# Kernel optimization log

Hardware: AMD Instinct MI355X
Metric: run time of the kernel (lower is better)

Reference implementation:

```python
import jax, jax.numpy as jnp
import numpy as np

NUM_GRAPHS = 64

def setup_inputs() -> dict:
    key = jax.random.key(0)
    ks = jax.random.split(key, 12)
    N, E, D, H = 100000, 1600000, 128, 128
    s = 0.05  # weight scale for numerical stability
    x = jax.random.normal(ks[0], (N, D), dtype=jnp.float32)
    edge_src = jax.random.randint(ks[1], (E,), 0, N, dtype=jnp.int32)
    edge_dst = jax.random.randint(ks[2], (E,), 0, N, dtype=jnp.int32)
    batch = jnp.sort(jax.random.randint(ks[3], (N,), 0, NUM_GRAPHS, dtype=jnp.int32))
    Wp = jax.random.normal(ks[4], (D, H), dtype=jnp.float32) * s
    bp = jnp.zeros((H,), dtype=jnp.float32)
    Wr = jax.random.normal(ks[5], (4, H, H), dtype=jnp.float32) * s
    br = jnp.zeros((4, H), dtype=jnp.float32)
    Wo0 = jax.random.normal(ks[6], (H + D, H), dtype=jnp.float32) * s
    bo0 = jnp.zeros((H,), dtype=jnp.float32)
    Wo1 = jax.random.normal(ks[7], (H, H), dtype=jnp.float32) * s
    bo1 = jnp.zeros((H,), dtype=jnp.float32)
    return dict(x=x, Wp=Wp, bp=bp, Wr=Wr, br=br, Wo0=Wo0, bo0=bo0, Wo1=Wo1, bo1=bo1,
                edge_src=edge_src, edge_dst=edge_dst, batch=batch)

def reference(x, Wp, bp, Wr, br, Wo0, bo0, Wo1, bo1, edge_src, edge_dst, batch):
    N = x.shape[0]
    # GCN normalization with self-loops: deg[i] = in_degree(i) + 1
    deg = 1.0 + jax.ops.segment_sum(jnp.ones_like(edge_dst, dtype=x.dtype), edge_dst, num_segments=N)
    dis = deg ** -0.5                      # [N]
    enorm = dis[edge_src] * dis[edge_dst]  # [E] edge coefficients
    self_norm = (dis * dis)[:, None]       # [N,1] self-loop coefficient

    def gcn(h, W, b):
        h = h @ W                                              # [N,out]
        msg = h[edge_src] * enorm[:, None]                     # [E,out] gather
        agg = jax.ops.segment_sum(msg, edge_dst, num_segments=N)  # scatter-add
        return agg + h * self_norm + b

    # projection (dropout is identity in this deterministic reference)
    h = jax.nn.relu(gcn(x, Wp, bp))
    # recurrent block, 1 training iteration of 4 layers
    for i in range(4):
        h = jax.nn.relu(gcn(h, Wr[i], br[i]))
    h = jnp.concatenate([h, x], axis=1)    # [N, H+D]
    h = jax.nn.relu(h)
    # output head
    h = jax.nn.relu(gcn(h, Wo0, bo0))
    h = jax.nn.relu(gcn(h, Wo1, bo1))
    # global mean pool over graphs
    sums = jax.ops.segment_sum(h, batch, num_segments=NUM_GRAPHS)
    cnt = jax.ops.segment_sum(jnp.ones((N,), dtype=h.dtype), batch, num_segments=NUM_GRAPHS)
    return sums / jnp.maximum(cnt, 1.0)[:, None]
```

## Files before the change

### kernel.cpp

```cpp
#include <hip/hip_runtime.h>

typedef __attribute__((ext_vector_type(8))) short short8;
typedef __attribute__((ext_vector_type(4))) float f32x4;
typedef __attribute__((ext_vector_type(4))) unsigned short us4;

__device__ __forceinline__ unsigned short f2bf(float f) {
  unsigned int u = __float_as_uint(f);
  u = u + 0x7fffu + ((u >> 16) & 1u);
  return (unsigned short)(u >> 16);
}
__device__ __forceinline__ float bf2f(unsigned short h) {
  return __uint_as_float(((unsigned int)h) << 16);
}
__device__ __forceinline__ int swz(int r, int k) {
  return (((r * 128 + k) * 2) ^ ((r & 7) << 4));
}

__global__ void k_deg(const int* __restrict__ edst, int* __restrict__ degi, int E) {
  int e = blockIdx.x * 256 + threadIdx.x;
  if (e < E) atomicAdd(&degi[edst[e]], 1);
}

__global__ void k_node(const int* __restrict__ degi, int* __restrict__ start,
                       float* __restrict__ dis, int* __restrict__ total, int N) {
  int tid = threadIdx.x;
  int i = blockIdx.x * 256 + tid;
  int d = (i < N) ? degi[i] : 0;
  __shared__ int sd[256];
  sd[tid] = d; __syncthreads();
  #pragma unroll
  for (int off = 1; off < 256; off <<= 1) {
    int v = (tid >= off) ? sd[tid - off] : 0;
    __syncthreads();
    sd[tid] += v;
    __syncthreads();
  }
  __shared__ int sbase;
  if (tid == 255) sbase = atomicAdd(total, sd[255]);
  __syncthreads();
  if (i < N) {
    start[i] = sbase + sd[tid] - d;
    dis[i] = rsqrtf(1.0f + (float)d);
  }
}

__global__ void k_fill(const int* __restrict__ esrc, const int* __restrict__ edst,
                       const int* __restrict__ start, int* __restrict__ cursor,
                       const float* __restrict__ dis, int* __restrict__ col,
                       float* __restrict__ wgt, int E) {
  int e = blockIdx.x * 256 + threadIdx.x;
  if (e >= E) return;
  int d = edst[e], s = esrc[e];
  int p = start[d] + atomicAdd(&cursor[d], 1);
  col[p] = s;
  wgt[p] = dis[s] * dis[d];
}

__global__ void k_wt(const float* __restrict__ Wp, const float* __restrict__ Wr,
                     const float* __restrict__ Wo0, const float* __restrict__ Wo1,
                     unsigned short* __restrict__ Whi, unsigned short* __restrict__ Wlo) {
  int idx = blockIdx.x * 256 + threadIdx.x;
  if (idx >= 8 * 16384) return;
  int m = idx >> 14, rem = idx & 16383;
  int c = rem >> 7, k = rem & 127;
  float v;
  if (m == 0)       v = Wp[k * 128 + c];
  else if (m <= 4)  v = Wr[(m - 1) * 16384 + k * 128 + c];
  else if (m == 5)  v = Wo0[k * 128 + c];
  else if (m == 6)  v = Wo0[(128 + k) * 128 + c];
  else              v = Wo1[k * 128 + c];
  unsigned short hh = f2bf(v);
  Whi[idx] = hh;
  Wlo[idx] = f2bf(v - bf2f(hh));
}

#define AHI_OFF 0
#define ALO_OFF 16384
#define WHI_OFF 32768
#define WLO_OFF 49152

template<bool ACC, bool RELU_A>
__global__ __launch_bounds__(256)
void k_gemm(const float* __restrict__ A, const unsigned short* __restrict__ Whi,
            const unsigned short* __restrict__ Wlo, unsigned short* __restrict__ TB, int N) {
  __shared__ __align__(16) char smem[65536];
  const int tid = threadIdx.x;
  const int grow = blockIdx.x * 64;
  const int cb = blockIdx.y * 64;

  #pragma unroll
  for (int it = 0; it < 4; ++it) {
    int id = it * 256 + tid;
    int r = id >> 4;
    int kp = (id & 15) * 8;
    int ga = grow + r; if (ga > N - 1) ga = N - 1;
    const float* ap = A + (size_t)ga * 128 + kp;
    float4 a0 = *(const float4*)ap;
    float4 a1 = *(const float4*)(ap + 4);
    if (RELU_A) {
      a0.x = fmaxf(a0.x, 0.f); a0.y = fmaxf(a0.y, 0.f); a0.z = fmaxf(a0.z, 0.f); a0.w = fmaxf(a0.w, 0.f);
      a1.x = fmaxf(a1.x, 0.f); a1.y = fmaxf(a1.y, 0.f); a1.z = fmaxf(a1.z, 0.f); a1.w = fmaxf(a1.w, 0.f);
    }
    {
      float fv[8] = {a0.x, a0.y, a0.z, a0.w, a1.x, a1.y, a1.z, a1.w};
      short8 hi, lo;
      #pragma unroll
      for (int q = 0; q < 8; ++q) {
        unsigned short hh = f2bf(fv[q]);
        hi[q] = (short)hh;
        lo[q] = (short)f2bf(fv[q] - bf2f(hh));
      }
      *(short8*)(smem + AHI_OFF + swz(r, kp)) = hi;
      *(short8*)(smem + ALO_OFF + swz(r, kp)) = lo;
    }
    size_t wo = (size_t)(cb + r) * 128 + kp;
    *(short8*)(smem + WHI_OFF + swz(r, kp)) = *(const short8*)(Whi + wo);
    *(short8*)(smem + WLO_OFF + swz(r, kp)) = *(const short8*)(Wlo + wo);
  }
  __syncthreads();

  const int l = tid & 63;
  const int w = tid >> 6;
  const int wr = (w >> 1) * 32;
  const int wc = (w & 1) * 32;
  const int lr = l & 15;
  const int lk = (l >> 4) * 8;

  f32x4 acc[2][2];
  #pragma unroll
  for (int i = 0; i < 2; ++i)
    #pragma unroll
    for (int j = 0; j < 2; ++j)
      acc[i][j] = (f32x4){0.f, 0.f, 0.f, 0.f};

  #pragma unroll
  for (int kk = 0; kk < 4; ++kk) {
    int k0 = kk * 32 + lk;
    short8 ahi[2], alo[2], bhi[2], blo[2];
    #pragma unroll
    for (int i = 0; i < 2; ++i) {
      int r = wr + i * 16 + lr;
      ahi[i] = *(const short8*)(smem + AHI_OFF + swz(r, k0));
      alo[i] = *(const short8*)(smem + ALO_OFF + swz(r, k0));
    }
    #pragma unroll
    for (int j = 0; j < 2; ++j) {
      int c = wc + j * 16 + lr;
      bhi[j] = *(const short8*)(smem + WHI_OFF + swz(c, k0));
      blo[j] = *(const short8*)(smem + WLO_OFF + swz(c, k0));
    }
    #pragma unroll
    for (int i = 0; i < 2; ++i)
      #pragma unroll
      for (int j = 0; j < 2; ++j) {
        acc[i][j] = __builtin_amdgcn_mfma_f32_16x16x32_bf16(ahi[i], bhi[j], acc[i][j], 0, 0, 0);
        acc[i][j] = __builtin_amdgcn_mfma_f32_16x16x32_bf16(ahi[i], blo[j], acc[i][j], 0, 0, 0);
        acc[i][j] = __builtin_amdgcn_mfma_f32_16x16x32_bf16(alo[i], bhi[j], acc[i][j], 0, 0, 0);
      }
  }

  #pragma unroll
  for (int i = 0; i < 2; ++i)
    #pragma unroll
    for (int j = 0; j < 2; ++j)
      #pragma unroll
      for (int r = 0; r < 4; ++r) {
        int row = grow + wr + i * 16 + (l >> 4) * 4 + r;
        int c = cb + wc + j * 16 + lr;
        if (row < N) {
          size_t idx = (size_t)row * 128 + c;
          float v = acc[i][j][r];
          if (ACC) v += bf2f(TB[idx]);
          TB[idx] = f2bf(v);
        }
      }
}

__global__ __launch_bounds__(256)
void k_agg(const unsigned short* __restrict__ tb, const int* __restrict__ col,
           const float* __restrict__ wgt, const int* __restrict__ start,
           const int* __restrict__ degi, const float* __restrict__ dis,
           const float* __restrict__ bias, float* __restrict__ hout, int N) {
  int node = blockIdx.x * 4 + (threadIdx.x >> 6);
  if (node >= N) return;
  int lane = threadIdx.x & 63;
  int half = lane >> 5;
  int fq = (lane & 31) * 4;

  float dsv = dis[node];
  float sn = dsv * dsv;
  f32x4 acc = (f32x4){0.f, 0.f, 0.f, 0.f};
  if (half == 0) {
    us4 sv = *(const us4*)(tb + (size_t)node * 128 + fq);
    float4 bv = *(const float4*)(bias + fq);
    acc[0] = bf2f(sv[0]) * sn + bv.x;
    acc[1] = bf2f(sv[1]) * sn + bv.y;
    acc[2] = bf2f(sv[2]) * sn + bv.z;
    acc[3] = bf2f(sv[3]) * sn + bv.w;
  }

#define LOADP(k, rr, ww) { int ii = 2 * (k) + half;                       \
    int ss = __shfl(ce, ii & 63); float wv = __shfl(we, ii & 63);         \
    ww = (ii < m) ? wv : 0.f;                                             \
    us4 u = *(const us4*)(tb + (size_t)ss * 128 + fq);                    \
    rr[0] = bf2f(u[0]); rr[1] = bf2f(u[1]);                               \
    rr[2] = bf2f(u[2]); rr[3] = bf2f(u[3]); }

  int s = start[node], d = degi[node];
  for (int base = 0; base < d; base += 64) {
    int m = min(64, d - base);
    int ce = 0; float we = 0.f;
    if (lane < m) { ce = col[s + base + lane]; we = wgt[s + base + lane]; }
    int npairs = (m + 1) >> 1;
    f32x4 p0, p1, p2, p3; float w0, w1, w2, w3;
    LOADP(0, p0, w0); LOADP(1, p1, w1); LOADP(2, p2, w2); LOADP(3, p3, w3);
    int q = 0;
    for (; q + 4 < npairs; q += 4) {
      acc += p0 * w0; LOADP(q + 4, p0, w0);
      acc += p1 * w1; LOADP(q + 5, p1, w1);
      acc += p2 * w2; LOADP(q + 6, p2, w2);
      acc += p3 * w3; LOADP(q + 7, p3, w3);
    }
    acc += p0 * w0; acc += p1 * w1; acc += p2 * w2; acc += p3 * w3;
  }
#undef LOADP

  acc[0] += __shfl_xor(acc[0], 32);
  acc[1] += __shfl_xor(acc[1], 32);
  acc[2] += __shfl_xor(acc[2], 32);
  acc[3] += __shfl_xor(acc[3], 32);

  if (half == 0) {
    f32x4 o;
    o[0] = fmaxf(acc[0], 0.f); o[1] = fmaxf(acc[1], 0.f);
    o[2] = fmaxf(acc[2], 0.f); o[3] = fmaxf(acc[3], 0.f);
    *(f32x4*)(hout + (size_t)node * 128 + fq) = o;
  }
}

__global__ void k_gb(const int* __restrict__ batch, int* __restrict__ gstart, int N) {
  int i = blockIdx.x * 256 + threadIdx.x;
  if (i >= N) return;
  int b = batch[i];
  int prev = (i == 0) ? -1 : batch[i - 1];
  if (b != prev) {
    for (int g = prev + 1; g <= b; ++g) gstart[g] = i;
  }
  if (i == N - 1) {
    for (int g = b + 1; g <= 64; ++g) gstart[g] = N;
  }
}

__global__ __launch_bounds__(512)
void k_pool1(const float* __restrict__ h, const int* __restrict__ gstart,
             float* __restrict__ part) {
  int g = blockIdx.x >> 2, c = blockIdx.x & 3;
  int lo = gstart[g], hi = gstart[g + 1];
  int cnt = hi - lo;
  int c0 = lo + (int)(((long long)cnt * c) >> 2);
  int c1 = lo + (int)(((long long)cnt * (c + 1)) >> 2);
  int r = threadIdx.x >> 7;
  int f = threadIdx.x & 127;
  float acc = 0.f;
  for (int i = c0 + r; i < c1; i += 4) acc += h[(size_t)i * 128 + f];
  __shared__ float s[4][128];
  s[r][f] = acc;
  __syncthreads();
  if (r == 0)
    part[(size_t)blockIdx.x * 128 + f] = s[0][f] + s[1][f] + s[2][f] + s[3][f];
}

__global__ void k_pool2(const float* __restrict__ part, const int* __restrict__ gstart,
                        float* __restrict__ out) {
  int g = blockIdx.x, f = threadIdx.x;
  int cnt = gstart[g + 1] - gstart[g];
  float s = part[(size_t)(g * 4 + 0) * 128 + f] + part[(size_t)(g * 4 + 1) * 128 + f]
          + part[(size_t)(g * 4 + 2) * 128 + f] + part[(size_t)(g * 4 + 3) * 128 + f];
  out[g * 128 + f] = s / (float)(cnt > 0 ? cnt : 1);
}

extern "C" void kernel_launch(void* const* d_in, const int* in_sizes, int n_in,
                              void* d_out, int out_size, void* d_ws, size_t ws_size,
                              hipStream_t stream) {
  const float* x   = (const float*)d_in[0];
  const float* Wp  = (const float*)d_in[1];
  const float* bp  = (const float*)d_in[2];
  const float* Wr  = (const float*)d_in[3];
  const float* br  = (const float*)d_in[4];
  const float* Wo0 = (const float*)d_in[5];
  const float* bo0 = (const float*)d_in[6];
  const float* Wo1 = (const float*)d_in[7];
  const float* bo1 = (const float*)d_in[8];
  const int* esrc  = (const int*)d_in[9];
  const int* edst  = (const int*)d_in[10];
  const int* batch = (const int*)d_in[11];
  const int E = in_sizes[9];
  const int N = in_sizes[11];
  float* out = (float*)d_out;

  char* wsp = (char*)d_ws;
  size_t off = 0;
  auto alloc = [&](size_t bytes) {
    void* p = wsp + off;
    off += (bytes + 255) & ~(size_t)255;
    return p;
  };
  unsigned short* tb = (unsigned short*)alloc((size_t)N * 128 * 2);
  float* h      = (float*)alloc((size_t)N * 128 * 4);
  int*   col    = (int*)alloc((size_t)E * 4);
  float* wgt    = (float*)alloc((size_t)E * 4);
  int*   start  = (int*)alloc((size_t)N * 4);
  int*   degi   = (int*)alloc((size_t)N * 4);
  int*   cursor = (int*)alloc((size_t)N * 4);
  float* dis    = (float*)alloc((size_t)N * 4);
  unsigned short* Whi = (unsigned short*)alloc((size_t)8 * 16384 * 2);
  unsigned short* Wlo = (unsigned short*)alloc((size_t)8 * 16384 * 2);
  int*   gstart = (int*)alloc(65 * 4);
  int*   total  = (int*)alloc(16);
  float* part   = (float*)cursor;

  hipMemsetAsync(degi,   0, (size_t)N * 4, stream);
  hipMemsetAsync(cursor, 0, (size_t)N * 4, stream);
  hipMemsetAsync(total,  0, 4, stream);

  k_deg <<<(E + 255) / 256, 256, 0, stream>>>(edst, degi, E);
  k_node<<<(N + 255) / 256, 256, 0, stream>>>(degi, start, dis, total, N);
  k_fill<<<(E + 255) / 256, 256, 0, stream>>>(esrc, edst, start, cursor, dis, col, wgt, E);
  k_wt  <<<512, 256, 0, stream>>>(Wp, Wr, Wo0, Wo1, Whi, Wlo);
  k_gb  <<<(N + 255) / 256, 256, 0, stream>>>(batch, gstart, N);

  dim3 ggrid((N + 63) / 64, 2);

  k_gemm<false, false><<<ggrid, 256, 0, stream>>>(x, Whi + 0 * 16384, Wlo + 0 * 16384, tb, N);
  k_agg<<<(N + 3) / 4, 256, 0, stream>>>(tb, col, wgt, start, degi, dis, bp, h, N);
  for (int i = 0; i < 4; ++i) {
    k_gemm<false, false><<<ggrid, 256, 0, stream>>>(h, Whi + (1 + i) * 16384, Wlo + (1 + i) * 16384, tb, N);
    k_agg<<<(N + 3) / 4, 256, 0, stream>>>(tb, col, wgt, start, degi, dis, br + i * 128, h, N);
  }
  k_gemm<false, false><<<ggrid, 256, 0, stream>>>(h, Whi + 5 * 16384, Wlo + 5 * 16384, tb, N);
  k_gemm<true,  true ><<<ggrid, 256, 0, stream>>>(x, Whi + 6 * 16384, Wlo + 6 * 16384, tb, N);
  k_agg<<<(N + 3) / 4, 256, 0, stream>>>(tb, col, wgt, start, degi, dis, bo0, h, N);
  k_gemm<false, false><<<ggrid, 256, 0, stream>>>(h, Whi + 7 * 16384, Wlo + 7 * 16384, tb, N);
  k_agg<<<(N + 3) / 4, 256, 0, stream>>>(tb, col, wgt, start, degi, dis, bo1, h, N);

  k_pool1<<<256, 512, 0, stream>>>(h, gstart, part);
  k_pool2<<<64, 128, 0, stream>>>(part, gstart, out);
}
```

Baseline: 995.6 us.

## Store hidden activations as bf16 and compute edge weights on the fly

Hidden activations between layers are now stored as bf16 instead of fp32. The GEMM gets a bf16-A path that copies A straight into LDS and drops the A-low MFMA term, which cuts LDS use and MFMA count. The per-edge weight array is removed; the aggregation recomputes each weight as dis[src]*dis[dst], saving the wgt writes in k_fill and the wgt reads in every layer at the cost of an extra gather from dis. Dropping the A-low term lowers precision relative to the split-bf16 scheme, and the pooled output now reads bf16 values.

```diff
diff --git a/kernel.cpp b/kernel.cpp
--- a/kernel.cpp
+++ b/kernel.cpp
@@ -46,14 +46,12 @@
 
 __global__ void k_fill(const int* __restrict__ esrc, const int* __restrict__ edst,
                        const int* __restrict__ start, int* __restrict__ cursor,
-                       const float* __restrict__ dis, int* __restrict__ col,
-                       float* __restrict__ wgt, int E) {
+                       int* __restrict__ col, int E) {
   int e = blockIdx.x * 256 + threadIdx.x;
   if (e >= E) return;
   int d = edst[e], s = esrc[e];
   int p = start[d] + atomicAdd(&cursor[d], 1);
   col[p] = s;
-  wgt[p] = dis[s] * dis[d];
 }
 
 __global__ void k_wt(const float* __restrict__ Wp, const float* __restrict__ Wr,
@@ -74,16 +72,15 @@
   Wlo[idx] = f2bf(v - bf2f(hh));
 }
 
-#define AHI_OFF 0
-#define ALO_OFF 16384
-#define WHI_OFF 32768
-#define WLO_OFF 49152
-
-template<bool ACC, bool RELU_A>
+template<bool ACC, bool RELU_A, bool ABF16>
 __global__ __launch_bounds__(256)
-void k_gemm(const float* __restrict__ A, const unsigned short* __restrict__ Whi,
+void k_gemm(const void* __restrict__ Av, const unsigned short* __restrict__ Whi,
             const unsigned short* __restrict__ Wlo, unsigned short* __restrict__ TB, int N) {
-  __shared__ __align__(16) char smem[65536];
+  constexpr int AHI_OFF = 0;
+  constexpr int WHI_OFF = 16384;
+  constexpr int WLO_OFF = 32768;
+  constexpr int ALO_OFF = 49152;
+  __shared__ __align__(16) char smem[ABF16 ? 49152 : 65536];
   const int tid = threadIdx.x;
   const int grow = blockIdx.x * 64;
   const int cb = blockIdx.y * 64;
@@ -94,14 +91,17 @@
     int r = id >> 4;
     int kp = (id & 15) * 8;
     int ga = grow + r; if (ga > N - 1) ga = N - 1;
-    const float* ap = A + (size_t)ga * 128 + kp;
-    float4 a0 = *(const float4*)ap;
-    float4 a1 = *(const float4*)(ap + 4);
-    if (RELU_A) {
-      a0.x = fmaxf(a0.x, 0.f); a0.y = fmaxf(a0.y, 0.f); a0.z = fmaxf(a0.z, 0.f); a0.w = fmaxf(a0.w, 0.f);
-      a1.x = fmaxf(a1.x, 0.f); a1.y = fmaxf(a1.y, 0.f); a1.z = fmaxf(a1.z, 0.f); a1.w = fmaxf(a1.w, 0.f);
-    }
-    {
+    if constexpr (ABF16) {
+      const unsigned short* ap = (const unsigned short*)Av + (size_t)ga * 128 + kp;
+      *(short8*)(smem + AHI_OFF + swz(r, kp)) = *(const short8*)ap;
+    } else {
+      const float* ap = (const float*)Av + (size_t)ga * 128 + kp;
+      float4 a0 = *(const float4*)ap;
+      float4 a1 = *(const float4*)(ap + 4);
+      if (RELU_A) {
+        a0.x = fmaxf(a0.x, 0.f); a0.y = fmaxf(a0.y, 0.f); a0.z = fmaxf(a0.z, 0.f); a0.w = fmaxf(a0.w, 0.f);
+        a1.x = fmaxf(a1.x, 0.f); a1.y = fmaxf(a1.y, 0.f); a1.z = fmaxf(a1.z, 0.f); a1.w = fmaxf(a1.w, 0.f);
+      }
       float fv[8] = {a0.x, a0.y, a0.z, a0.w, a1.x, a1.y, a1.z, a1.w};
       short8 hi, lo;
       #pragma unroll
@@ -141,7 +141,8 @@
     for (int i = 0; i < 2; ++i) {
       int r = wr + i * 16 + lr;
       ahi[i] = *(const short8*)(smem + AHI_OFF + swz(r, k0));
-      alo[i] = *(const short8*)(smem + ALO_OFF + swz(r, k0));
+      if constexpr (!ABF16)
+        alo[i] = *(const short8*)(smem + ALO_OFF + swz(r, k0));
     }
     #pragma unroll
     for (int j = 0; j < 2; ++j) {
@@ -155,7 +156,8 @@
       for (int j = 0; j < 2; ++j) {
         acc[i][j] = __builtin_amdgcn_mfma_f32_16x16x32_bf16(ahi[i], bhi[j], acc[i][j], 0, 0, 0);
         acc[i][j] = __builtin_amdgcn_mfma_f32_16x16x32_bf16(ahi[i], blo[j], acc[i][j], 0, 0, 0);
-        acc[i][j] = __builtin_amdgcn_mfma_f32_16x16x32_bf16(alo[i], bhi[j], acc[i][j], 0, 0, 0);
+        if constexpr (!ABF16)
+          acc[i][j] = __builtin_amdgcn_mfma_f32_16x16x32_bf16(alo[i], bhi[j], acc[i][j], 0, 0, 0);
       }
   }
 
@@ -178,9 +180,9 @@
 
 __global__ __launch_bounds__(256)
 void k_agg(const unsigned short* __restrict__ tb, const int* __restrict__ col,
-           const float* __restrict__ wgt, const int* __restrict__ start,
-           const int* __restrict__ degi, const float* __restrict__ dis,
-           const float* __restrict__ bias, float* __restrict__ hout, int N) {
+           const int* __restrict__ start, const int* __restrict__ degi,
+           const float* __restrict__ dis, const float* __restrict__ bias,
+           unsigned short* __restrict__ hb, int N) {
   int node = blockIdx.x * 4 + (threadIdx.x >> 6);
   if (node >= N) return;
   int lane = threadIdx.x & 63;
@@ -210,7 +212,10 @@
   for (int base = 0; base < d; base += 64) {
     int m = min(64, d - base);
     int ce = 0; float we = 0.f;
-    if (lane < m) { ce = col[s + base + lane]; we = wgt[s + base + lane]; }
+    if (lane < m) {
+      ce = col[s + base + lane];
+      we = dis[ce] * dsv;
+    }
     int npairs = (m + 1) >> 1;
     f32x4 p0, p1, p2, p3; float w0, w1, w2, w3;
     LOADP(0, p0, w0); LOADP(1, p1, w1); LOADP(2, p2, w2); LOADP(3, p3, w3);
@@ -231,10 +236,10 @@
   acc[3] += __shfl_xor(acc[3], 32);
 
   if (half == 0) {
-    f32x4 o;
-    o[0] = fmaxf(acc[0], 0.f); o[1] = fmaxf(acc[1], 0.f);
-    o[2] = fmaxf(acc[2], 0.f); o[3] = fmaxf(acc[3], 0.f);
-    *(f32x4*)(hout + (size_t)node * 128 + fq) = o;
+    us4 o;
+    o[0] = f2bf(fmaxf(acc[0], 0.f)); o[1] = f2bf(fmaxf(acc[1], 0.f));
+    o[2] = f2bf(fmaxf(acc[2], 0.f)); o[3] = f2bf(fmaxf(acc[3], 0.f));
+    *(us4*)(hb + (size_t)node * 128 + fq) = o;
   }
 }
 
@@ -252,7 +257,7 @@
 }
 
 __global__ __launch_bounds__(512)
-void k_pool1(const float* __restrict__ h, const int* __restrict__ gstart,
+void k_pool1(const unsigned short* __restrict__ hb, const int* __restrict__ gstart,
              float* __restrict__ part) {
   int g = blockIdx.x >> 2, c = blockIdx.x & 3;
   int lo = gstart[g], hi = gstart[g + 1];
@@ -262,7 +267,7 @@
   int r = threadIdx.x >> 7;
   int f = threadIdx.x & 127;
   float acc = 0.f;
-  for (int i = c0 + r; i < c1; i += 4) acc += h[(size_t)i * 128 + f];
+  for (int i = c0 + r; i < c1; i += 4) acc += bf2f(hb[(size_t)i * 128 + f]);
   __shared__ float s[4][128];
   s[r][f] = acc;
   __syncthreads();
@@ -306,9 +311,8 @@
     return p;
   };
   unsigned short* tb = (unsigned short*)alloc((size_t)N * 128 * 2);
-  float* h      = (float*)alloc((size_t)N * 128 * 4);
+  unsigned short* hb = (unsigned short*)alloc((size_t)N * 128 * 2);
   int*   col    = (int*)alloc((size_t)E * 4);
-  float* wgt    = (float*)alloc((size_t)E * 4);
   int*   start  = (int*)alloc((size_t)N * 4);
   int*   degi   = (int*)alloc((size_t)N * 4);
   int*   cursor = (int*)alloc((size_t)N * 4);
@@ -325,24 +329,24 @@
 
   k_deg <<<(E + 255) / 256, 256, 0, stream>>>(edst, degi, E);
   k_node<<<(N + 255) / 256, 256, 0, stream>>>(degi, start, dis, total, N);
-  k_fill<<<(E + 255) / 256, 256, 0, stream>>>(esrc, edst, start, cursor, dis, col, wgt, E);
+  k_fill<<<(E + 255) / 256, 256, 0, stream>>>(esrc, edst, start, cursor, col, E);
   k_wt  <<<512, 256, 0, stream>>>(Wp, Wr, Wo0, Wo1, Whi, Wlo);
   k_gb  <<<(N + 255) / 256, 256, 0, stream>>>(batch, gstart, N);
 
   dim3 ggrid((N + 63) / 64, 2);
 
-  k_gemm<false, false><<<ggrid, 256, 0, stream>>>(x, Whi + 0 * 16384, Wlo + 0 * 16384, tb, N);
-  k_agg<<<(N + 3) / 4, 256, 0, stream>>>(tb, col, wgt, start, degi, dis, bp, h, N);
+  k_gemm<false, false, false><<<ggrid, 256, 0, stream>>>(x, Whi + 0 * 16384, Wlo + 0 * 16384, tb, N);
+  k_agg<<<(N + 3) / 4, 256, 0, stream>>>(tb, col, start, degi, dis, bp, hb, N);
   for (int i = 0; i < 4; ++i) {
-    k_gemm<false, false><<<ggrid, 256, 0, stream>>>(h, Whi + (1 + i) * 16384, Wlo + (1 + i) * 16384, tb, N);
-    k_agg<<<(N + 3) / 4, 256, 0, stream>>>(tb, col, wgt, start, degi, dis, br + i * 128, h, N);
-  }
-  k_gemm<false, false><<<ggrid, 256, 0, stream>>>(h, Whi + 5 * 16384, Wlo + 5 * 16384, tb, N);
-  k_gemm<true,  true ><<<ggrid, 256, 0, stream>>>(x, Whi + 6 * 16384, Wlo + 6 * 16384, tb, N);
-  k_agg<<<(N + 3) / 4, 256, 0, stream>>>(tb, col, wgt, start, degi, dis, bo0, h, N);
-  k_gemm<false, false><<<ggrid, 256, 0, stream>>>(h, Whi + 7 * 16384, Wlo + 7 * 16384, tb, N);
-  k_agg<<<(N + 3) / 4, 256, 0, stream>>>(tb, col, wgt, start, degi, dis, bo1, h, N);
-
-  k_pool1<<<256, 512, 0, stream>>>(h, gstart, part);
+    k_gemm<false, false, true><<<ggrid, 256, 0, stream>>>(hb, Whi + (1 + i) * 16384, Wlo + (1 + i) * 16384, tb, N);
+    k_agg<<<(N + 3) / 4, 256, 0, stream>>>(tb, col, start, degi, dis, br + i * 128, hb, N);
+  }
+  k_gemm<false, false, true ><<<ggrid, 256, 0, stream>>>(hb, Whi + 5 * 16384, Wlo + 5 * 16384, tb, N);
+  k_gemm<true,  true,  false><<<ggrid, 256, 0, stream>>>(x, Whi + 6 * 16384, Wlo + 6 * 16384, tb, N);
+  k_agg<<<(N + 3) / 4, 256, 0, stream>>>(tb, col, start, degi, dis, bo0, hb, N);
+  k_gemm<false, false, true><<<ggrid, 256, 0, stream>>>(hb, Whi + 7 * 16384, Wlo + 7 * 16384, tb, N);
+  k_agg<<<(N + 3) / 4, 256, 0, stream>>>(tb, col, start, degi, dis, bo1, hb, N);
+
+  k_pool1<<<256, 512, 0, stream>>>(hb, gstart, part);
   k_pool2<<<64, 128, 0, stream>>>(part, gstart, out);
 }
```

After: 988.4 us. No clear change (-0.7%).
